# Performance work log

Measured on AMD Instinct MI355X. Metric: run time of the kernel, lower is better.

## Reference

```python
import jax, jax.numpy as jnp
import numpy as np

B, L, D, H = 8, 1024, 1024, 16
HD = D // H  # head dim = 64


def _split_heads(x):
    # [B, L, D] -> [B, H, L, HD]
    return x.reshape(B, L, H, HD).transpose(0, 2, 1, 3)


def setup_inputs() -> dict:
    key = jax.random.key(0)
    ks = jax.random.split(key, 16)
    s = 0.02
    inp = {
        "hidden_states": jax.random.normal(ks[0], (B, L, D), jnp.float32),
        "attention_mask": jnp.zeros((B, 1, 1, L), jnp.float32),
        "source_embedding": jax.random.normal(ks[1], (B, L, D), jnp.float32),
        # self-attention projections
        "Wq": jax.random.normal(ks[2], (D, D), jnp.float32) * s,
        "bq": jnp.zeros((D,), jnp.float32),
        "Wk": jax.random.normal(ks[3], (D, D), jnp.float32) * s,
        "bk": jnp.zeros((D,), jnp.float32),
        "Wv": jax.random.normal(ks[4], (D, D), jnp.float32) * s,
        "bv": jnp.zeros((D,), jnp.float32),
        # SourceAttendsSubthread projections (query on hidden, key on source)
        "Wq2": jax.random.normal(ks[5], (D, D), jnp.float32) * s,
        "bq2": jnp.zeros((D,), jnp.float32),
        "Wk2": jax.random.normal(ks[6], (D, D), jnp.float32) * s,
        "bk2": jnp.zeros((D,), jnp.float32),
    }
    return inp


def reference(hidden_states, attention_mask, source_embedding,
              Wq, bq, Wk, bk, Wv, bv, Wq2, bq2, Wk2, bk2):
    scale = 1.0 / jnp.sqrt(jnp.asarray(HD, hidden_states.dtype))
    q = _split_heads(hidden_states @ Wq + bq)          # [B,H,L,HD]
    k = _split_heads(hidden_states @ Wk + bk)
    v = _split_heads(hidden_states @ Wv + bv)
    q2 = _split_heads(hidden_states @ Wq2 + bq2)
    k2 = _split_heads(source_embedding @ Wk2 + bk2)
    scores = jnp.einsum('bhqd,bhkd->bhqk', q, k) * scale
    scores = scores + jnp.einsum('bhqd,bhkd->bhqk', q2, k2) * scale
    scores = scores + attention_mask                   # broadcast [B,1,1,L]
    probs = jax.nn.softmax(scores, axis=-1)            # dropout is identity (p=0 / eval)
    ctx = jnp.einsum('bhqk,bhkd->bhqd', probs, v)      # [B,H,L,HD]
    return ctx.transpose(0, 2, 1, 3).reshape(B, L, D)
```

## Files before the change

### kernel.cpp

```cpp
#include <hip/hip_runtime.h>
#include <hip/hip_bf16.h>
#include <stdint.h>

#define Bn 8
#define Ln 1024
#define Dn 1024
#define Hn 16
#define HDn 64
#define Mn (Bn*Ln)
#define Kn 1024

typedef __attribute__((ext_vector_type(8))) __bf16 bf16x8;
typedef __attribute__((ext_vector_type(4))) float f32x4;

__device__ __forceinline__ unsigned short f2bf(float f) {
    unsigned int u = __float_as_uint(f);
    unsigned int r = (u + 0x7fff + ((u >> 16) & 1)) >> 16;
    return (unsigned short)r;
}

__device__ __forceinline__ void gload_lds16(void* lds, const void* g) {
    __builtin_amdgcn_global_load_lds(
        (const __attribute__((address_space(1))) unsigned int*)g,
        (__attribute__((address_space(3))) unsigned int*)lds,
        16, 0, 0);
}

__global__ void cvt_bf16_kernel(const float* __restrict__ h,
                                const float* __restrict__ s,
                                unsigned short* __restrict__ ho,
                                unsigned short* __restrict__ so) {
    const float* in = blockIdx.y ? s : h;
    unsigned short* out = blockIdx.y ? so : ho;
    size_t i = ((size_t)blockIdx.x * blockDim.x + threadIdx.x) * 4;
    float4 f = *(const float4*)(in + i);
    ushort4 o;
    o.x = f2bf(f.x); o.y = f2bf(f.y); o.z = f2bf(f.z); o.w = f2bf(f.w);
    *(ushort4*)(out + i) = o;
}

__global__ void transpose_w_kernel(const float* __restrict__ Wq,
                                   const float* __restrict__ Wk,
                                   const float* __restrict__ Wq2,
                                   const float* __restrict__ Wk2,
                                   const float* __restrict__ Wv,
                                   unsigned short* __restrict__ wcat4,
                                   unsigned short* __restrict__ wtv) {
    __shared__ float tile[32][33];
    const float* W; unsigned short* Wt;
    switch (blockIdx.z) {
        case 0: W = Wq;  Wt = wcat4;                 break;
        case 1: W = Wk;  Wt = wcat4 + 1024 * 1024;   break;
        case 2: W = Wq2; Wt = wcat4 + 2048 * 1024;   break;
        case 3: W = Wk2; Wt = wcat4 + 3072 * 1024;   break;
        default:W = Wv;  Wt = wtv;                   break;
    }
    int bx = blockIdx.x, by = blockIdx.y;
    int tx = threadIdx.x, ty = threadIdx.y;
    int col = bx * 32 + tx;
    for (int i = 0; i < 32; i += 8)
        tile[ty + i][tx] = W[(size_t)(by * 32 + ty + i) * Dn + col];
    __syncthreads();
    int ok = by * 32 + tx;
    for (int i = 0; i < 32; i += 8)
        Wt[(size_t)(bx * 32 + ty + i) * Kn + ok] = f2bf(tile[tx][ty + i]);
}

__device__ __forceinline__ void gemm_mainloop(const unsigned short* __restrict__ A,
                                              const unsigned short* __restrict__ Bt,
                                              unsigned short* As, unsigned short* Bs,
                                              int m0, int n0, f32x4 acc[4][4]) {
    int t = threadIdx.x;
    int lane = t & 63, wave = t >> 6;
    int wm = (wave >> 1) * 64, wn = (wave & 1) * 64;
    int lrow = lane & 15, lquad = lane >> 4;
    int arow = t >> 2;
    int ac = ((t & 3) ^ (arow & 3)) * 8;
    int rs = lrow & 3;

    for (int k0 = 0; k0 < Kn; k0 += 32) {
        gload_lds16(&As[t * 8],         A  + (size_t)(m0 + arow) * Kn + k0 + ac);
        gload_lds16(&As[(t + 256) * 8], A  + (size_t)(m0 + 64 + arow) * Kn + k0 + ac);
        gload_lds16(&Bs[t * 8],         Bt + (size_t)(n0 + arow) * Kn + k0 + ac);
        gload_lds16(&Bs[(t + 256) * 8], Bt + (size_t)(n0 + 64 + arow) * Kn + k0 + ac);
        __syncthreads();
        bf16x8 af[4], bfr[4];
        for (int i = 0; i < 4; i++)
            af[i] = *(const bf16x8*)&As[(wm + i * 16 + lrow) * 32 + (lquad ^ rs) * 8];
        for (int j = 0; j < 4; j++)
            bfr[j] = *(const bf16x8*)&Bs[(wn + j * 16 + lrow) * 32 + (lquad ^ rs) * 8];
        for (int i = 0; i < 4; i++)
            for (int j = 0; j < 4; j++)
                acc[i][j] = __builtin_amdgcn_mfma_f32_16x16x32_bf16(af[i], bfr[j], acc[i][j], 0, 0, 0);
        __syncthreads();
    }
}

__launch_bounds__(256, 2)
__global__ void gemm_qkq2k2_kernel(const unsigned short* __restrict__ hb,
                                   const unsigned short* __restrict__ sb,
                                   const unsigned short* __restrict__ Bt,
                                   const float* __restrict__ bq,
                                   const float* __restrict__ bk,
                                   const float* __restrict__ bq2,
                                   const float* __restrict__ bk2,
                                   unsigned short* __restrict__ qbuf,
                                   unsigned short* __restrict__ kbuf,
                                   unsigned short* __restrict__ q2buf,
                                   unsigned short* __restrict__ k2buf) {
    __shared__ __align__(16) unsigned short As[128 * 32];
    __shared__ __align__(16) unsigned short Bs[128 * 32];
    int m0 = blockIdx.y * 128, n0 = blockIdx.x * 128;
    int region = n0 >> 10;
    const unsigned short* A = (region == 3) ? sb : hb;
    f32x4 acc[4][4] = {};
    gemm_mainloop(A, Bt, As, Bs, m0, n0, acc);

    const float* bp = region == 0 ? bq : region == 1 ? bk : region == 2 ? bq2 : bk2;
    unsigned short* dp = region == 0 ? qbuf : region == 1 ? kbuf : region == 2 ? q2buf : k2buf;
    float sc = (region == 0 || region == 2) ? 0.125f : 1.0f;

    int t = threadIdx.x;
    int lane = t & 63, wave = t >> 6;
    int wm = (wave >> 1) * 64, wn = (wave & 1) * 64;
    int lrow = lane & 15, lquad = lane >> 4;
    for (int j = 0; j < 4; j++) {
        int gn = (n0 & 1023) + wn + j * 16 + lrow;
        float bv = bp[gn];
        int h = gn >> 6, hd = gn & 63;
        for (int i = 0; i < 4; i++)
            for (int r = 0; r < 4; r++) {
                int gm = m0 + wm + i * 16 + lquad * 4 + r;
                int b = gm >> 10, ll = gm & 1023;
                dp[((size_t)(b * Hn + h) * Ln + ll) * HDn + hd] = f2bf((acc[i][j][r] + bv) * sc);
            }
    }
}

__launch_bounds__(256, 2)
__global__ void gemm_vT_kernel(const unsigned short* __restrict__ Wt,
                               const unsigned short* __restrict__ Xb,
                               const float* __restrict__ bias,
                               unsigned short* __restrict__ vtbuf) {
    __shared__ __align__(16) unsigned short As[128 * 32];
    __shared__ __align__(16) unsigned short Bs[128 * 32];
    int m0 = blockIdx.y * 128;
    int n0 = blockIdx.x * 128;
    f32x4 acc[4][4] = {};
    gemm_mainloop(Wt, Xb, As, Bs, m0, n0, acc);

    int t = threadIdx.x;
    int lane = t & 63, wave = t >> 6;
    int wm = (wave >> 1) * 64, wn = (wave & 1) * 64;
    int lrow = lane & 15, lquad = lane >> 4;
    for (int j = 0; j < 4; j++) {
        int gn = n0 + wn + j * 16 + lrow;
        int b = gn >> 10, l = gn & 1023;
        for (int i = 0; i < 4; i++)
            for (int r = 0; r < 4; r++) {
                int gm = m0 + wm + i * 16 + lquad * 4 + r;
                int h = gm >> 6, hd = gm & 63;
                vtbuf[((size_t)(b * Hn + h) * HDn + hd) * Ln + l] = f2bf(acc[i][j][r] + bias[gm]);
            }
    }
}

__launch_bounds__(256, 3)
__global__ void attn_kernel(const unsigned short* __restrict__ qb,
                            const unsigned short* __restrict__ kb,
                            const unsigned short* __restrict__ q2b,
                            const unsigned short* __restrict__ k2b,
                            const unsigned short* __restrict__ vtb,
                            const float* __restrict__ mask,
                            float* __restrict__ out) {
    __shared__ __align__(16) unsigned short Ks[64 * 64];
    __shared__ __align__(16) unsigned short K2s[64 * 64];
    __shared__ __align__(16) unsigned short VTs[64 * 64];
    __shared__ __align__(16) unsigned short Ps[4 * 32 * 64];

    int bh = blockIdx.x;
    int qt = blockIdx.y;
    int b = bh >> 4;
    int t = threadIdx.x;
    int lane = t & 63, wave = t >> 6;
    int lrow = lane & 15, lquad = lane >> 4;
    int qbase = qt * 128 + wave * 32;

    bf16x8 qf[2][2], q2f[2][2];
    for (int rt = 0; rt < 2; rt++)
        for (int kk = 0; kk < 2; kk++) {
            size_t off = ((size_t)bh * Ln + qbase + rt * 16 + lrow) * HDn + kk * 32 + lquad * 8;
            qf[rt][kk]  = *(const bf16x8*)(qb + off);
            q2f[rt][kk] = *(const bf16x8*)(q2b + off);
        }

    f32x4 O[2][4] = {};
    f32x4 lsum[2] = {};

    int srow = t >> 3;
    int sc8 = ((t & 7) ^ (srow & 7)) * 8;
    const float* maskb = mask + (size_t)b * Ln;
    int rph = lrow & 7;
    unsigned short* pw = &Ps[wave * 32 * 64];

    for (int kt = 0; kt < 16; kt++) {
        int key0 = kt * 64;
        gload_lds16(&Ks[t * 8],          kb  + ((size_t)bh * Ln + key0 + srow) * HDn + sc8);
        gload_lds16(&Ks[(t + 256) * 8],  kb  + ((size_t)bh * Ln + key0 + 32 + srow) * HDn + sc8);
        gload_lds16(&K2s[t * 8],         k2b + ((size_t)bh * Ln + key0 + srow) * HDn + sc8);
        gload_lds16(&K2s[(t + 256) * 8], k2b + ((size_t)bh * Ln + key0 + 32 + srow) * HDn + sc8);
        gload_lds16(&VTs[t * 8],         vtb + ((size_t)bh * HDn + srow) * Ln + key0 + sc8);
        gload_lds16(&VTs[(t + 256) * 8], vtb + ((size_t)bh * HDn + 32 + srow) * Ln + key0 + sc8);
        __syncthreads();

        f32x4 S[2][4];
        for (int j = 0; j < 4; j++) {
            float mk = maskb[key0 + j * 16 + lrow];
            S[0][j] = (f32x4){mk, mk, mk, mk};
            S[1][j] = S[0][j];
        }
        for (int kk = 0; kk < 2; kk++) {
            for (int j = 0; j < 4; j++) {
                bf16x8 kf = *(const bf16x8*)&Ks[(j * 16 + lrow) * 64 + ((kk * 4 + lquad) ^ rph) * 8];
                S[0][j] = __builtin_amdgcn_mfma_f32_16x16x32_bf16(qf[0][kk], kf, S[0][j], 0, 0, 0);
                S[1][j] = __builtin_amdgcn_mfma_f32_16x16x32_bf16(qf[1][kk], kf, S[1][j], 0, 0, 0);
            }
            for (int j = 0; j < 4; j++) {
                bf16x8 kf = *(const bf16x8*)&K2s[(j * 16 + lrow) * 64 + ((kk * 4 + lquad) ^ rph) * 8];
                S[0][j] = __builtin_amdgcn_mfma_f32_16x16x32_bf16(q2f[0][kk], kf, S[0][j], 0, 0, 0);
                S[1][j] = __builtin_amdgcn_mfma_f32_16x16x32_bf16(q2f[1][kk], kf, S[1][j], 0, 0, 0);
            }
        }

        for (int rt = 0; rt < 2; rt++)
            for (int j = 0; j < 4; j++)
                for (int r = 0; r < 4; r++) {
                    float e = __expf(S[rt][j][r]);
                    lsum[rt][r] += e;
                    int pr = rt * 16 + lquad * 4 + r;
                    int cw = (j * 2 + (lrow >> 3)) ^ (pr & 7);
                    pw[pr * 64 + cw * 8 + (lrow & 7)] = f2bf(e);
                }

        for (int kk = 0; kk < 2; kk++) {
            bf16x8 pf0 = *(const bf16x8*)&pw[lrow * 64 + ((kk * 4 + lquad) ^ rph) * 8];
            bf16x8 pf1 = *(const bf16x8*)&pw[(16 + lrow) * 64 + ((kk * 4 + lquad) ^ rph) * 8];
            for (int j = 0; j < 4; j++) {
                bf16x8 vf = *(const bf16x8*)&VTs[(j * 16 + lrow) * 64 + ((kk * 4 + lquad) ^ rph) * 8];
                O[0][j] = __builtin_amdgcn_mfma_f32_16x16x32_bf16(pf0, vf, O[0][j], 0, 0, 0);
                O[1][j] = __builtin_amdgcn_mfma_f32_16x16x32_bf16(pf1, vf, O[1][j], 0, 0, 0);
            }
        }
        __syncthreads();
    }

    for (int rt = 0; rt < 2; rt++)
        for (int r = 0; r < 4; r++) {
            float s = lsum[rt][r];
            for (int d = 1; d < 16; d <<= 1)
                s += __shfl_xor(s, d, 64);
            lsum[rt][r] = s;
        }

    int h = bh & 15;
    for (int rt = 0; rt < 2; rt++)
        for (int r = 0; r < 4; r++) {
            float rl = 1.0f / lsum[rt][r];
            int ql = qbase + rt * 16 + lquad * 4 + r;
            for (int j = 0; j < 4; j++)
                out[((size_t)b * Ln + ql) * Dn + h * HDn + j * 16 + lrow] = O[rt][j][r] * rl;
        }
}

extern "C" void kernel_launch(void* const* d_in, const int* in_sizes, int n_in,
                              void* d_out, int out_size, void* d_ws, size_t ws_size,
                              hipStream_t stream) {
    const float* hidden = (const float*)d_in[0];
    const float* mask   = (const float*)d_in[1];
    const float* source = (const float*)d_in[2];
    const float* Wq  = (const float*)d_in[3];
    const float* bq  = (const float*)d_in[4];
    const float* Wk  = (const float*)d_in[5];
    const float* bk  = (const float*)d_in[6];
    const float* Wv  = (const float*)d_in[7];
    const float* bv  = (const float*)d_in[8];
    const float* Wq2 = (const float*)d_in[9];
    const float* bq2 = (const float*)d_in[10];
    const float* Wk2 = (const float*)d_in[11];
    const float* bk2 = (const float*)d_in[12];
    float* out = (float*)d_out;

    char* ws = (char*)d_ws;
    const size_t act_sz = (size_t)Mn * Dn * 2;
    const size_t w_sz   = (size_t)Kn * Dn * 2;
    unsigned short* hb    = (unsigned short*)ws; ws += act_sz;
    unsigned short* sb    = (unsigned short*)ws; ws += act_sz;
    unsigned short* wcat4 = (unsigned short*)ws; ws += 4 * w_sz;
    unsigned short* wtv   = (unsigned short*)ws; ws += w_sz;
    unsigned short* qbuf  = (unsigned short*)ws; ws += act_sz;
    unsigned short* kbuf  = (unsigned short*)ws; ws += act_sz;
    unsigned short* q2buf = (unsigned short*)ws; ws += act_sz;
    unsigned short* k2buf = (unsigned short*)ws; ws += act_sz;
    unsigned short* vtbuf = (unsigned short*)ws; ws += act_sz;

    dim3 cgrid((Mn * Dn / 4) / 256, 2);
    cvt_bf16_kernel<<<cgrid, 256, 0, stream>>>(hidden, source, hb, sb);

    dim3 tgrid(32, 32, 5), tblk(32, 8);
    transpose_w_kernel<<<tgrid, tblk, 0, stream>>>(Wq, Wk, Wq2, Wk2, Wv, wcat4, wtv);

    dim3 g1(4096 / 128, Mn / 128);
    gemm_qkq2k2_kernel<<<g1, 256, 0, stream>>>(hb, sb, wcat4, bq, bk, bq2, bk2,
                                               qbuf, kbuf, q2buf, k2buf);
    dim3 g3(Mn / 128, Dn / 128);
    gemm_vT_kernel<<<g3, 256, 0, stream>>>(wtv, hb, bv, vtbuf);

    dim3 agrid(Bn * Hn, Ln / 128);
    attn_kernel<<<agrid, 256, 0, stream>>>(qbuf, kbuf, q2buf, k2buf, vtbuf, mask, out);
}
```

Before: 352.3 us.

## Change GEMM LDS swizzle layout and merge QKQ2K2 and V-transpose GEMMs into one launch

Reorganizes the LDS tile for the shared GEMM mainloop so each 64-element LDS row holds two 32-wide K rows, with an 8-way XOR swizzle. This is meant to cut bank conflicts on the 16-byte fragment reads, and global addresses are precomputed outside the K loop. It also fuses the two projection GEMM launches into a single 2560-block kernel that branches on block index. That removes one launch and the tail gap between the two kernels, at the cost of a divergent per-block code path.

Measured after the change: 351.7 us. Within noise of the previous version (-0.2%).

```diff
diff --git a/kernel.cpp b/kernel.cpp
--- a/kernel.cpp
+++ b/kernel.cpp
@@ -74,21 +74,30 @@
     int lane = t & 63, wave = t >> 6;
     int wm = (wave >> 1) * 64, wn = (wave & 1) * 64;
     int lrow = lane & 15, lquad = lane >> 4;
-    int arow = t >> 2;
-    int ac = ((t & 3) ^ (arow & 3)) * 8;
-    int rs = lrow & 3;
+
+    int q2 = (t & 7) ^ ((t >> 3) & 7);
+    int srow = ((t >> 3) << 1) | (q2 >> 2);
+    int scol = (q2 & 3) * 8;
+    const unsigned short* ap0 = A  + (size_t)(m0 + srow) * Kn + scol;
+    const unsigned short* ap1 = A  + (size_t)(m0 + 64 + srow) * Kn + scol;
+    const unsigned short* bp0 = Bt + (size_t)(n0 + srow) * Kn + scol;
+    const unsigned short* bp1 = Bt + (size_t)(n0 + 64 + srow) * Kn + scol;
+
+    int rslot8 = ((((lrow & 1) << 2) | lquad) ^ ((lrow >> 1) & 7)) * 8;
+    int rbaseA = ((wm >> 1) + (lrow >> 1)) * 64;
+    int rbaseB = ((wn >> 1) + (lrow >> 1)) * 64;
 
     for (int k0 = 0; k0 < Kn; k0 += 32) {
-        gload_lds16(&As[t * 8],         A  + (size_t)(m0 + arow) * Kn + k0 + ac);
-        gload_lds16(&As[(t + 256) * 8], A  + (size_t)(m0 + 64 + arow) * Kn + k0 + ac);
-        gload_lds16(&Bs[t * 8],         Bt + (size_t)(n0 + arow) * Kn + k0 + ac);
-        gload_lds16(&Bs[(t + 256) * 8], Bt + (size_t)(n0 + 64 + arow) * Kn + k0 + ac);
+        gload_lds16(&As[t * 8],         ap0 + k0);
+        gload_lds16(&As[(t + 256) * 8], ap1 + k0);
+        gload_lds16(&Bs[t * 8],         bp0 + k0);
+        gload_lds16(&Bs[(t + 256) * 8], bp1 + k0);
         __syncthreads();
         bf16x8 af[4], bfr[4];
         for (int i = 0; i < 4; i++)
-            af[i] = *(const bf16x8*)&As[(wm + i * 16 + lrow) * 32 + (lquad ^ rs) * 8];
+            af[i] = *(const bf16x8*)&As[rbaseA + i * 8 * 64 + rslot8];
         for (int j = 0; j < 4; j++)
-            bfr[j] = *(const bf16x8*)&Bs[(wn + j * 16 + lrow) * 32 + (lquad ^ rs) * 8];
+            bfr[j] = *(const bf16x8*)&Bs[rbaseB + j * 8 * 64 + rslot8];
         for (int i = 0; i < 4; i++)
             for (int j = 0; j < 4; j++)
                 acc[i][j] = __builtin_amdgcn_mfma_f32_16x16x32_bf16(af[i], bfr[j], acc[i][j], 0, 0, 0);
@@ -97,71 +106,65 @@
 }
 
 __launch_bounds__(256, 2)
-__global__ void gemm_qkq2k2_kernel(const unsigned short* __restrict__ hb,
-                                   const unsigned short* __restrict__ sb,
-                                   const unsigned short* __restrict__ Bt,
-                                   const float* __restrict__ bq,
-                                   const float* __restrict__ bk,
-                                   const float* __restrict__ bq2,
-                                   const float* __restrict__ bk2,
-                                   unsigned short* __restrict__ qbuf,
-                                   unsigned short* __restrict__ kbuf,
-                                   unsigned short* __restrict__ q2buf,
-                                   unsigned short* __restrict__ k2buf) {
+__global__ void gemm_all_kernel(const unsigned short* __restrict__ hb,
+                                const unsigned short* __restrict__ sb,
+                                const unsigned short* __restrict__ wcat4,
+                                const unsigned short* __restrict__ wtv,
+                                const float* __restrict__ bq,
+                                const float* __restrict__ bk,
+                                const float* __restrict__ bq2,
+                                const float* __restrict__ bk2,
+                                const float* __restrict__ bv,
+                                unsigned short* __restrict__ qbuf,
+                                unsigned short* __restrict__ kbuf,
+                                unsigned short* __restrict__ q2buf,
+                                unsigned short* __restrict__ k2buf,
+                                unsigned short* __restrict__ vtbuf) {
     __shared__ __align__(16) unsigned short As[128 * 32];
     __shared__ __align__(16) unsigned short Bs[128 * 32];
-    int m0 = blockIdx.y * 128, n0 = blockIdx.x * 128;
-    int region = n0 >> 10;
-    const unsigned short* A = (region == 3) ? sb : hb;
-    f32x4 acc[4][4] = {};
-    gemm_mainloop(A, Bt, As, Bs, m0, n0, acc);
-
-    const float* bp = region == 0 ? bq : region == 1 ? bk : region == 2 ? bq2 : bk2;
-    unsigned short* dp = region == 0 ? qbuf : region == 1 ? kbuf : region == 2 ? q2buf : k2buf;
-    float sc = (region == 0 || region == 2) ? 0.125f : 1.0f;
-
+    int bid = blockIdx.x;
     int t = threadIdx.x;
     int lane = t & 63, wave = t >> 6;
     int wm = (wave >> 1) * 64, wn = (wave & 1) * 64;
     int lrow = lane & 15, lquad = lane >> 4;
-    for (int j = 0; j < 4; j++) {
-        int gn = (n0 & 1023) + wn + j * 16 + lrow;
-        float bv = bp[gn];
-        int h = gn >> 6, hd = gn & 63;
-        for (int i = 0; i < 4; i++)
-            for (int r = 0; r < 4; r++) {
-                int gm = m0 + wm + i * 16 + lquad * 4 + r;
-                int b = gm >> 10, ll = gm & 1023;
-                dp[((size_t)(b * Hn + h) * Ln + ll) * HDn + hd] = f2bf((acc[i][j][r] + bv) * sc);
-            }
-    }
-}
-
-__launch_bounds__(256, 2)
-__global__ void gemm_vT_kernel(const unsigned short* __restrict__ Wt,
-                               const unsigned short* __restrict__ Xb,
-                               const float* __restrict__ bias,
-                               unsigned short* __restrict__ vtbuf) {
-    __shared__ __align__(16) unsigned short As[128 * 32];
-    __shared__ __align__(16) unsigned short Bs[128 * 32];
-    int m0 = blockIdx.y * 128;
-    int n0 = blockIdx.x * 128;
     f32x4 acc[4][4] = {};
-    gemm_mainloop(Wt, Xb, As, Bs, m0, n0, acc);
-
-    int t = threadIdx.x;
-    int lane = t & 63, wave = t >> 6;
-    int wm = (wave >> 1) * 64, wn = (wave & 1) * 64;
-    int lrow = lane & 15, lquad = lane >> 4;
-    for (int j = 0; j < 4; j++) {
-        int gn = n0 + wn + j * 16 + lrow;
-        int b = gn >> 10, l = gn & 1023;
-        for (int i = 0; i < 4; i++)
-            for (int r = 0; r < 4; r++) {
-                int gm = m0 + wm + i * 16 + lquad * 4 + r;
-                int h = gm >> 6, hd = gm & 63;
-                vtbuf[((size_t)(b * Hn + h) * HDn + hd) * Ln + l] = f2bf(acc[i][j][r] + bias[gm]);
-            }
+
+    if (bid < 2048) {
+        int n0 = (bid & 31) * 128, m0 = (bid >> 5) * 128;
+        int region = n0 >> 10;
+        const unsigned short* A = (region == 3) ? sb : hb;
+        gemm_mainloop(A, wcat4, As, Bs, m0, n0, acc);
+
+        const float* bp = region == 0 ? bq : region == 1 ? bk : region == 2 ? bq2 : bk2;
+        unsigned short* dp = region == 0 ? qbuf : region == 1 ? kbuf : region == 2 ? q2buf : k2buf;
+        float sc = (region == 0 || region == 2) ? 0.125f : 1.0f;
+        for (int j = 0; j < 4; j++) {
+            int gn = (n0 & 1023) + wn + j * 16 + lrow;
+            float bv_ = bp[gn];
+            int h = gn >> 6, hd = gn & 63;
+            for (int i = 0; i < 4; i++)
+                for (int r = 0; r < 4; r++) {
+                    int gm = m0 + wm + i * 16 + lquad * 4 + r;
+                    int b = gm >> 10, ll = gm & 1023;
+                    dp[((size_t)(b * Hn + h) * Ln + ll) * HDn + hd] = f2bf((acc[i][j][r] + bv_) * sc);
+                }
+        }
+    } else {
+        int b2 = bid - 2048;
+        int n0 = (b2 & 63) * 128;
+        int m0 = (b2 >> 6) * 128;
+        gemm_mainloop(wtv, hb, As, Bs, m0, n0, acc);
+
+        for (int j = 0; j < 4; j++) {
+            int gn = n0 + wn + j * 16 + lrow;
+            int b = gn >> 10, l = gn & 1023;
+            for (int i = 0; i < 4; i++)
+                for (int r = 0; r < 4; r++) {
+                    int gm = m0 + wm + i * 16 + lquad * 4 + r;
+                    int h = gm >> 6, hd = gm & 63;
+                    vtbuf[((size_t)(b * Hn + h) * HDn + hd) * Ln + l] = f2bf(acc[i][j][r] + bv[gm]);
+                }
+        }
     }
 }
 
@@ -309,11 +312,9 @@
     dim3 tgrid(32, 32, 5), tblk(32, 8);
     transpose_w_kernel<<<tgrid, tblk, 0, stream>>>(Wq, Wk, Wq2, Wk2, Wv, wcat4, wtv);
 
-    dim3 g1(4096 / 128, Mn / 128);
-    gemm_qkq2k2_kernel<<<g1, 256, 0, stream>>>(hb, sb, wcat4, bq, bk, bq2, bk2,
-                                               qbuf, kbuf, q2buf, k2buf);
-    dim3 g3(Mn / 128, Dn / 128);
-    gemm_vT_kernel<<<g3, 256, 0, stream>>>(wtv, hb, bv, vtbuf);
+    gemm_all_kernel<<<2560, 256, 0, stream>>>(hb, sb, wcat4, wtv,
+                                              bq, bk, bq2, bk2, bv,
+                                              qbuf, kbuf, q2buf, k2buf, vtbuf);
 
     dim3 agrid(Bn * Hn, Ln / 128);
     attn_kernel<<<agrid, 256, 0, stream>>>(qbuf, kbuf, q2buf, k2buf, vtbuf, mask, out);
```
